# Kernel tuning notes

Hardware: AMD Instinct MI355X
Metric: run time of the kernel (lower is better)

Reference implementation:

```python
import jax, jax.numpy as jnp
import numpy as np

HIDDEN = 128
GRID = 8
NEIGH = 4.0
CELL = NEIGH / GRID


def setup_inputs() -> dict:
    key = jax.random.key(0)
    k1, k2, k3, k4 = jax.random.split(key, 4)
    B, N = 64, 64
    hidden_states = jax.random.normal(k1, (B, N, HIDDEN), dtype=jnp.float32)
    positions = jax.random.normal(k2, (B, N, 2), dtype=jnp.float32)
    fan_in = HIDDEN * GRID * GRID
    bound = 1.0 / np.sqrt(fan_in)
    W = jax.random.uniform(k3, (HIDDEN, fan_in), minval=-bound, maxval=bound, dtype=jnp.float32)
    b = jax.random.uniform(k4, (HIDDEN,), minval=-bound, maxval=bound, dtype=jnp.float32)
    return {"hidden_states": hidden_states, "positions": positions, "W": W, "b": b}


def reference(hidden_states, positions, W, b):
    B, N, H = hidden_states.shape
    G, G2 = GRID, GRID * GRID
    # rel[b, i, j] = positions[b, j] - positions[b, i]  (offset of neighbor j in agent i's frame)
    rel = positions[:, None, :, :] - positions[:, :, None, :]  # [B, N, N, 2]
    # torch .long() truncates toward zero; jnp astype(int32) does the same, and after
    # clamping to [0, G-1] this matches the original exactly.
    gx = ((rel[..., 0] + NEIGH / 2) / CELL).astype(jnp.int32).clip(0, G - 1)
    gy = ((rel[..., 1] + NEIGH / 2) / CELL).astype(jnp.int32).clip(0, G - 1)
    cell = gx * G + gy  # [B, N(i), N(j)] flat grid-cell index (gx-major, matching view order)
    # Exclude self (j == i) from pooling.
    not_self = (1.0 - jnp.eye(N, dtype=hidden_states.dtype))  # [N(i), N(j)]
    onehot = jax.nn.one_hot(cell, G2, dtype=hidden_states.dtype) * not_self[None, :, :, None]
    # Scatter-add neighbor hidden states into each agent's grid: [B, N(i), G2, H]
    grid = jnp.einsum('bijc,bjh->bich', onehot, hidden_states)
    grid_flat = grid.reshape(B, N, G2 * H)  # (gx, gy, h) flatten order == torch .view
    pooled = grid_flat @ W.T + b  # [B, N, H]
    return pooled
```

## Files before the change

kernel.cpp:

```cpp
#include <hip/hip_runtime.h>
#include <hip/hip_bf16.h>
#include <stdint.h>


typedef __attribute__((ext_vector_type(8))) short bf16x8;
typedef __attribute__((ext_vector_type(4))) float f32x4;
typedef unsigned int u32;

#define NCHUNK 8
#define CPB 8

__device__ inline unsigned short bf16bits(float x) {
    __hip_bfloat16 h = __float2bfloat16(x);
    return *reinterpret_cast<unsigned short*>(&h);
}

__global__ __launch_bounds__(512)
void gp_wconv(const float* __restrict__ W, __hip_bfloat16* __restrict__ Wb)
{
    __shared__ __attribute__((aligned(16))) __hip_bfloat16 Wl[128][136];
    const int c = blockIdx.x, t = threadIdx.x;
    #pragma unroll
    for (int q = 0; q < 8; ++q) {
        int flat = q * 512 + t;
        int ho = flat >> 5, k4 = flat & 31;
        float4 v = *(const float4*)(W + (size_t)ho * 8192 + c * 128 + k4 * 4);
        __hip_bfloat16* d = &Wl[ho][k4 * 4];
        d[0] = __float2bfloat16(v.x); d[1] = __float2bfloat16(v.y);
        d[2] = __float2bfloat16(v.z); d[3] = __float2bfloat16(v.w);
    }
    __syncthreads();
    #pragma unroll
    for (int q = 0; q < 4; ++q) {
        int flat = q * 512 + t;
        int hg = flat >> 7, ho = flat & 127;
        bf16x8 v = *(const bf16x8*)&Wl[ho][hg * 8];
        *(bf16x8*)(Wb + (size_t)c * 16384 + (size_t)flat * 8) = v;
    }
}

__global__ __launch_bounds__(256, 2)
void gp_main(const float* __restrict__ hid, const float* __restrict__ pos,
             const __hip_bfloat16* __restrict__ Wb, float* __restrict__ partial)
{
    __shared__ __attribute__((aligned(16))) __hip_bfloat16 Hs[16 * 64 * 8];
    __shared__ u32 zscr[4][1024];
    __shared__ unsigned char cellt[64 * 64];
    __shared__ float ps[128];

    const int t = threadIdx.x;
    const int b = blockIdx.x & 63, chunk = blockIdx.x >> 6;
    const int w = t >> 6, lane = t & 63;
    const int l15 = lane & 15, kg = lane >> 4;

    if (t < 128) ps[t] = pos[(size_t)b * 128 + t];
    __syncthreads();

    #pragma unroll
    for (int q = 0; q < 16; ++q) {
        int idx = q * 256 + t;
        int i = idx >> 6, j = idx & 63;
        float rx = ps[j * 2 + 0] - ps[i * 2 + 0];
        float ry = ps[j * 2 + 1] - ps[i * 2 + 1];
        int gx = (int)((rx + 2.0f) * 2.0f);
        int gy = (int)((ry + 2.0f) * 2.0f);
        gx = gx < 0 ? 0 : (gx > 7 ? 7 : gx);
        gy = gy < 0 ? 0 : (gy > 7 ? 7 : gy);
        cellt[idx] = (i == j) ? 255 : (unsigned char)(gx * 8 + gy);
    }
    #pragma unroll
    for (int q = 0; q < 4; ++q) {
        int idx = q * 256 + t;
        int hg = idx >> 6, j = idx & 63;
        const float* src = hid + ((size_t)b * 64 + j) * 128 + hg * 8;
        float4 v0 = *(const float4*)src;
        float4 v1 = *(const float4*)(src + 4);
        __hip_bfloat16* d = &Hs[(hg * 64 + j) * 8];
        d[0] = __float2bfloat16(v0.x); d[1] = __float2bfloat16(v0.y);
        d[2] = __float2bfloat16(v0.z); d[3] = __float2bfloat16(v0.w);
        d[4] = __float2bfloat16(v1.x); d[5] = __float2bfloat16(v1.y);
        d[6] = __float2bfloat16(v1.z); d[7] = __float2bfloat16(v1.w);
    }
    __syncthreads();

    bf16x8 a[4][4];
    #pragma unroll
    for (int jt = 0; jt < 4; ++jt)
        #pragma unroll
        for (int ks = 0; ks < 4; ++ks) {
            int hg = ks * 4 + kg;
            a[jt][ks] = *(const bf16x8*)&Hs[(hg * 64 + jt * 16 + l15) * 8];
        }
    uint2 cs[4][2];
    #pragma unroll
    for (int mt = 0; mt < 4; ++mt)
        #pragma unroll
        for (int ks2 = 0; ks2 < 2; ++ks2)
            cs[mt][ks2] = *(const uint2*)&cellt[(mt * 16 + l15) * 64 + ks2 * 32 + kg * 8];

    f32x4 acc[4][2];
    #pragma unroll
    for (int mt = 0; mt < 4; ++mt) {
        acc[mt][0] = (f32x4){0.f, 0.f, 0.f, 0.f};
        acc[mt][1] = (f32x4){0.f, 0.f, 0.f, 0.f};
    }

    u32* zw = &zscr[w][0];

    bf16x8 wf[2][4][2];
    {
        const __hip_bfloat16* wc = Wb + (size_t)(chunk * CPB) * 16384;
        #pragma unroll
        for (int ks = 0; ks < 4; ++ks)
            #pragma unroll
            for (int fh = 0; fh < 2; ++fh)
                wf[0][ks][fh] = *(const bf16x8*)(wc +
                    ((size_t)(ks * 4 + kg) * 128 + w * 32 + fh * 16 + l15) * 8);
    }

    #pragma unroll
    for (int cc = 0; cc < CPB; ++cc) {
        const int p = cc & 1;
        const int c = chunk * CPB + cc;

        if (cc + 1 < CPB) {
            const __hip_bfloat16* wc = Wb + (size_t)(c + 1) * 16384;
            #pragma unroll
            for (int ks = 0; ks < 4; ++ks)
                #pragma unroll
                for (int fh = 0; fh < 2; ++fh)
                    wf[p ^ 1][ks][fh] = *(const bf16x8*)(wc +
                        ((size_t)(ks * 4 + kg) * 128 + w * 32 + fh * 16 + l15) * 8);
        }

        f32x4 z[4][2];
        #pragma unroll
        for (int jt = 0; jt < 4; ++jt) {
            z[jt][0] = (f32x4){0.f, 0.f, 0.f, 0.f};
            z[jt][1] = (f32x4){0.f, 0.f, 0.f, 0.f};
        }
        #pragma unroll
        for (int ks = 0; ks < 4; ++ks)
            #pragma unroll
            for (int jt = 0; jt < 4; ++jt) {
                z[jt][0] = __builtin_amdgcn_mfma_f32_16x16x32_bf16(a[jt][ks], wf[p][ks][0], z[jt][0], 0, 0, 0);
                z[jt][1] = __builtin_amdgcn_mfma_f32_16x16x32_bf16(a[jt][ks], wf[p][ks][1], z[jt][1], 0, 0, 0);
            }

        #pragma unroll
        for (int jt = 0; jt < 4; ++jt)
            #pragma unroll
            for (int fh = 0; fh < 2; ++fh) {
                u32 p0 = (u32)bf16bits(z[jt][fh][0]) | ((u32)bf16bits(z[jt][fh][1]) << 16);
                u32 p1 = (u32)bf16bits(z[jt][fh][2]) | ((u32)bf16bits(z[jt][fh][3]) << 16);
                int X = ((jt * 2 + (kg >> 1)) & 3) << 3;
                int a32 = (((jt * 8 + kg * 2) * 32) + fh * 16 + l15) ^ X;
                zw[a32] = p0;
                zw[a32 + 32] = p1;
            }

        bf16x8 b2[2][2];
        #pragma unroll
        for (int ks2 = 0; ks2 < 2; ++ks2)
            #pragma unroll
            for (int fh = 0; fh < 2; ++fh) {
                int base = (((ks2 * 16 + kg * 4) * 32) + fh * 16 + l15) ^ (kg << 3);
                union { u32 wd[4]; bf16x8 v; } r;
                r.wd[0] = zw[base];
                r.wd[1] = zw[base + 32];
                r.wd[2] = zw[base + 64];
                r.wd[3] = zw[base + 96];
                b2[ks2][fh] = r.v;
            }

        #pragma unroll
        for (int mt = 0; mt < 4; ++mt) {
            #pragma unroll
            for (int ks2 = 0; ks2 < 2; ++ks2) {
                union { u32 wd[4]; bf16x8 v; } m;
                u32 s0 = cs[mt][ks2].x, s1 = cs[mt][ks2].y;
                #pragma unroll
                for (int k = 0; k < 4; ++k) {
                    u32 s = (k < 2) ? s0 : s1;
                    u32 b0 = (s >> ((k & 1) * 16)) & 0xFFu;
                    u32 b1 = (s >> ((k & 1) * 16 + 8)) & 0xFFu;
                    m.wd[k] = (b0 == (u32)c ? 0x3F80u : 0u) | (b1 == (u32)c ? 0x3F800000u : 0u);
                }
                acc[mt][0] = __builtin_amdgcn_mfma_f32_16x16x32_bf16(m.v, b2[ks2][0], acc[mt][0], 0, 0, 0);
                acc[mt][1] = __builtin_amdgcn_mfma_f32_16x16x32_bf16(m.v, b2[ks2][1], acc[mt][1], 0, 0, 0);
            }
        }
    }

    float* pb = partial + (((size_t)chunk * 64 + b) * 64) * 128;
    #pragma unroll
    for (int mt = 0; mt < 4; ++mt)
        #pragma unroll
        for (int fh = 0; fh < 2; ++fh)
            #pragma unroll
            for (int r = 0; r < 4; ++r) {
                int i = mt * 16 + kg * 4 + r;
                int ho = w * 32 + fh * 16 + l15;
                pb[(size_t)i * 128 + ho] = acc[mt][fh][r];
            }
}

__global__ __launch_bounds__(512)
void gp_reduce(const float* __restrict__ partial, const float* __restrict__ bias,
               float* __restrict__ out)
{
    int gid = blockIdx.x * 512 + threadIdx.x;
    int ho4 = gid & 31;
    float4 a = *(const float4*)(bias + ho4 * 4);
    #pragma unroll
    for (int ch = 0; ch < NCHUNK; ++ch) {
        float4 v = *(const float4*)(partial + (size_t)ch * 524288 + (size_t)gid * 4);
        a.x += v.x; a.y += v.y; a.z += v.z; a.w += v.w;
    }
    *(float4*)(out + (size_t)gid * 4) = a;
}

extern "C" void kernel_launch(void* const* d_in, const int* in_sizes, int n_in,
                              void* d_out, int out_size, void* d_ws, size_t ws_size,
                              hipStream_t stream)
{
    const float* hid  = (const float*)d_in[0];
    const float* pos  = (const float*)d_in[1];
    const float* W    = (const float*)d_in[2];
    const float* bias = (const float*)d_in[3];
    float* out = (float*)d_out;

    __hip_bfloat16* Wb = (__hip_bfloat16*)d_ws;
    float* partial = (float*)((char*)d_ws + (size_t)2097152);

    hipLaunchKernelGGL(gp_wconv,  dim3(64),          dim3(512), 0, stream, W, Wb);
    hipLaunchKernelGGL(gp_main,   dim3(NCHUNK * 64), dim3(256), 0, stream, hid, pos, Wb, partial);
    hipLaunchKernelGGL(gp_reduce, dim3(256),         dim3(512), 0, stream, partial, bias, out);
}
```

Baseline: 38.42 us.

## Split main kernel into single-wave blocks and hoist per-batch prep into prep kernel

Per-batch cell-index computation and hidden-state bf16 conversion move out of the main kernel into a combined prep kernel that also converts W, finer-grained. The main kernel now runs one wave per block (4096 blocks, chunk count doubled to 16), reading bf16 hidden states and cell tables from global memory, with no block-level syncs and no W double-buffering. This aims to raise parallelism and remove the redundant per-block prep. In exchange, the reduce pass reads twice as many partials and the main kernel loses its software prefetch of W.

```diff
diff --git a/kernel.cpp b/kernel.cpp
--- a/kernel.cpp
+++ b/kernel.cpp
@@ -7,96 +7,104 @@
 typedef __attribute__((ext_vector_type(4))) float f32x4;
 typedef unsigned int u32;
 
-#define NCHUNK 8
-#define CPB 8
+#define NCHUNK 16
+#define CPB 4
 
 __device__ inline unsigned short bf16bits(float x) {
     __hip_bfloat16 h = __float2bfloat16(x);
     return *reinterpret_cast<unsigned short*>(&h);
 }
 
-__global__ __launch_bounds__(512)
-void gp_wconv(const float* __restrict__ W, __hip_bfloat16* __restrict__ Wb)
-{
-    __shared__ __attribute__((aligned(16))) __hip_bfloat16 Wl[128][136];
-    const int c = blockIdx.x, t = threadIdx.x;
-    #pragma unroll
-    for (int q = 0; q < 8; ++q) {
-        int flat = q * 512 + t;
-        int ho = flat >> 5, k4 = flat & 31;
-        float4 v = *(const float4*)(W + (size_t)ho * 8192 + c * 128 + k4 * 4);
-        __hip_bfloat16* d = &Wl[ho][k4 * 4];
-        d[0] = __float2bfloat16(v.x); d[1] = __float2bfloat16(v.y);
-        d[2] = __float2bfloat16(v.z); d[3] = __float2bfloat16(v.w);
-    }
-    __syncthreads();
-    #pragma unroll
-    for (int q = 0; q < 4; ++q) {
-        int flat = q * 512 + t;
-        int hg = flat >> 7, ho = flat & 127;
-        bf16x8 v = *(const bf16x8*)&Wl[ho][hg * 8];
-        *(bf16x8*)(Wb + (size_t)c * 16384 + (size_t)flat * 8) = v;
-    }
-}
-
-__global__ __launch_bounds__(256, 2)
-void gp_main(const float* __restrict__ hid, const float* __restrict__ pos,
-             const __hip_bfloat16* __restrict__ Wb, float* __restrict__ partial)
-{
-    __shared__ __attribute__((aligned(16))) __hip_bfloat16 Hs[16 * 64 * 8];
-    __shared__ u32 zscr[4][1024];
-    __shared__ unsigned char cellt[64 * 64];
-    __shared__ float ps[128];
-
-    const int t = threadIdx.x;
-    const int b = blockIdx.x & 63, chunk = blockIdx.x >> 6;
-    const int w = t >> 6, lane = t & 63;
+__global__ __launch_bounds__(256)
+void gp_prep(const float* __restrict__ W, const float* __restrict__ pos,
+             const float* __restrict__ hid,
+             __hip_bfloat16* __restrict__ Wb,
+             unsigned char* __restrict__ cellt_g,
+             __hip_bfloat16* __restrict__ Hb)
+{
+    const int bid = blockIdx.x, t = threadIdx.x;
+    if (bid < 256) {
+        __shared__ __attribute__((aligned(16))) __hip_bfloat16 Wl[32][136];
+        const int c = bid >> 2, q = bid & 3;
+        #pragma unroll
+        for (int it = 0; it < 4; ++it) {
+            int idx = it * 256 + t;
+            int r = idx >> 5, k4 = idx & 31;
+            float4 v = *(const float4*)(W + (size_t)(q * 32 + r) * 8192 + c * 128 + k4 * 4);
+            __hip_bfloat16* d = &Wl[r][k4 * 4];
+            d[0] = __float2bfloat16(v.x); d[1] = __float2bfloat16(v.y);
+            d[2] = __float2bfloat16(v.z); d[3] = __float2bfloat16(v.w);
+        }
+        __syncthreads();
+        #pragma unroll
+        for (int it = 0; it < 2; ++it) {
+            int idx = it * 256 + t;
+            int hg = idx >> 5, hol = idx & 31;
+            bf16x8 v = *(const bf16x8*)&Wl[hol][hg * 8];
+            *(bf16x8*)(Wb + (size_t)c * 16384 + hg * 1024 + (q * 32 + hol) * 8) = v;
+        }
+    } else if (bid < 320) {
+        __shared__ float ps[128];
+        const int b = bid - 256;
+        if (t < 128) ps[t] = pos[(size_t)b * 128 + t];
+        __syncthreads();
+        #pragma unroll
+        for (int qq = 0; qq < 16; ++qq) {
+            int idx = qq * 256 + t;
+            int i = idx >> 6, j = idx & 63;
+            float rx = ps[j * 2 + 0] - ps[i * 2 + 0];
+            float ry = ps[j * 2 + 1] - ps[i * 2 + 1];
+            int gx = (int)((rx + 2.0f) * 2.0f);
+            int gy = (int)((ry + 2.0f) * 2.0f);
+            gx = gx < 0 ? 0 : (gx > 7 ? 7 : gx);
+            gy = gy < 0 ? 0 : (gy > 7 ? 7 : gy);
+            cellt_g[(size_t)b * 4096 + idx] =
+                (i == j) ? 255 : (unsigned char)(gx * 8 + gy);
+        }
+    } else {
+        const int b = bid - 320;
+        #pragma unroll
+        for (int qq = 0; qq < 8; ++qq) {
+            int idx = qq * 256 + t;
+            float4 v = *(const float4*)(hid + (size_t)b * 8192 + idx * 4);
+            union { unsigned short us[4]; uint2 u; } pk;
+            pk.us[0] = bf16bits(v.x); pk.us[1] = bf16bits(v.y);
+            pk.us[2] = bf16bits(v.z); pk.us[3] = bf16bits(v.w);
+            *(uint2*)(Hb + (size_t)b * 8192 + idx * 4) = pk.u;
+        }
+    }
+}
+
+__global__ __launch_bounds__(64, 4)
+void gp_main(const __hip_bfloat16* __restrict__ Hb,
+             const unsigned char* __restrict__ cellt_g,
+             const __hip_bfloat16* __restrict__ Wb,
+             float* __restrict__ partial)
+{
+    __shared__ u32 zscr[1024];
+
+    const int x = blockIdx.x;
+    const int w = x & 3;
+    const int b = (x >> 2) & 63;
+    const int chunk = x >> 8;
+    const int lane = threadIdx.x;
     const int l15 = lane & 15, kg = lane >> 4;
 
-    if (t < 128) ps[t] = pos[(size_t)b * 128 + t];
-    __syncthreads();
-
-    #pragma unroll
-    for (int q = 0; q < 16; ++q) {
-        int idx = q * 256 + t;
-        int i = idx >> 6, j = idx & 63;
-        float rx = ps[j * 2 + 0] - ps[i * 2 + 0];
-        float ry = ps[j * 2 + 1] - ps[i * 2 + 1];
-        int gx = (int)((rx + 2.0f) * 2.0f);
-        int gy = (int)((ry + 2.0f) * 2.0f);
-        gx = gx < 0 ? 0 : (gx > 7 ? 7 : gx);
-        gy = gy < 0 ? 0 : (gy > 7 ? 7 : gy);
-        cellt[idx] = (i == j) ? 255 : (unsigned char)(gx * 8 + gy);
-    }
-    #pragma unroll
-    for (int q = 0; q < 4; ++q) {
-        int idx = q * 256 + t;
-        int hg = idx >> 6, j = idx & 63;
-        const float* src = hid + ((size_t)b * 64 + j) * 128 + hg * 8;
-        float4 v0 = *(const float4*)src;
-        float4 v1 = *(const float4*)(src + 4);
-        __hip_bfloat16* d = &Hs[(hg * 64 + j) * 8];
-        d[0] = __float2bfloat16(v0.x); d[1] = __float2bfloat16(v0.y);
-        d[2] = __float2bfloat16(v0.z); d[3] = __float2bfloat16(v0.w);
-        d[4] = __float2bfloat16(v1.x); d[5] = __float2bfloat16(v1.y);
-        d[6] = __float2bfloat16(v1.z); d[7] = __float2bfloat16(v1.w);
-    }
-    __syncthreads();
+    uint2 cs[4][2];
+    #pragma unroll
+    for (int mt = 0; mt < 4; ++mt)
+        #pragma unroll
+        for (int ks2 = 0; ks2 < 2; ++ks2)
+            cs[mt][ks2] = *(const uint2*)(cellt_g + (size_t)b * 4096 +
+                                          (mt * 16 + l15) * 64 + ks2 * 32 + kg * 8);
 
     bf16x8 a[4][4];
     #pragma unroll
     for (int jt = 0; jt < 4; ++jt)
         #pragma unroll
-        for (int ks = 0; ks < 4; ++ks) {
-            int hg = ks * 4 + kg;
-            a[jt][ks] = *(const bf16x8*)&Hs[(hg * 64 + jt * 16 + l15) * 8];
-        }
-    uint2 cs[4][2];
-    #pragma unroll
-    for (int mt = 0; mt < 4; ++mt)
-        #pragma unroll
-        for (int ks2 = 0; ks2 < 2; ++ks2)
-            cs[mt][ks2] = *(const uint2*)&cellt[(mt * 16 + l15) * 64 + ks2 * 32 + kg * 8];
+        for (int ks = 0; ks < 4; ++ks)
+            a[jt][ks] = *(const bf16x8*)(Hb + (size_t)b * 8192 +
+                                         (jt * 16 + l15) * 128 + (ks * 4 + kg) * 8);
 
     f32x4 acc[4][2];
     #pragma unroll
@@ -105,33 +113,17 @@
         acc[mt][1] = (f32x4){0.f, 0.f, 0.f, 0.f};
     }
 
-    u32* zw = &zscr[w][0];
-
-    bf16x8 wf[2][4][2];
-    {
-        const __hip_bfloat16* wc = Wb + (size_t)(chunk * CPB) * 16384;
+    #pragma unroll
+    for (int cc = 0; cc < CPB; ++cc) {
+        const int c = chunk * CPB + cc;
+
+        bf16x8 wf[4][2];
         #pragma unroll
         for (int ks = 0; ks < 4; ++ks)
             #pragma unroll
             for (int fh = 0; fh < 2; ++fh)
-                wf[0][ks][fh] = *(const bf16x8*)(wc +
-                    ((size_t)(ks * 4 + kg) * 128 + w * 32 + fh * 16 + l15) * 8);
-    }
-
-    #pragma unroll
-    for (int cc = 0; cc < CPB; ++cc) {
-        const int p = cc & 1;
-        const int c = chunk * CPB + cc;
-
-        if (cc + 1 < CPB) {
-            const __hip_bfloat16* wc = Wb + (size_t)(c + 1) * 16384;
-            #pragma unroll
-            for (int ks = 0; ks < 4; ++ks)
-                #pragma unroll
-                for (int fh = 0; fh < 2; ++fh)
-                    wf[p ^ 1][ks][fh] = *(const bf16x8*)(wc +
-                        ((size_t)(ks * 4 + kg) * 128 + w * 32 + fh * 16 + l15) * 8);
-        }
+                wf[ks][fh] = *(const bf16x8*)(Wb + (size_t)c * 16384 +
+                    ((ks * 4 + kg) * 128 + w * 32 + fh * 16 + l15) * 8);
 
         f32x4 z[4][2];
         #pragma unroll
@@ -143,8 +135,8 @@
         for (int ks = 0; ks < 4; ++ks)
             #pragma unroll
             for (int jt = 0; jt < 4; ++jt) {
-                z[jt][0] = __builtin_amdgcn_mfma_f32_16x16x32_bf16(a[jt][ks], wf[p][ks][0], z[jt][0], 0, 0, 0);
-                z[jt][1] = __builtin_amdgcn_mfma_f32_16x16x32_bf16(a[jt][ks], wf[p][ks][1], z[jt][1], 0, 0, 0);
+                z[jt][0] = __builtin_amdgcn_mfma_f32_16x16x32_bf16(a[jt][ks], wf[ks][0], z[jt][0], 0, 0, 0);
+                z[jt][1] = __builtin_amdgcn_mfma_f32_16x16x32_bf16(a[jt][ks], wf[ks][1], z[jt][1], 0, 0, 0);
             }
 
         #pragma unroll
@@ -155,8 +147,8 @@
                 u32 p1 = (u32)bf16bits(z[jt][fh][2]) | ((u32)bf16bits(z[jt][fh][3]) << 16);
                 int X = ((jt * 2 + (kg >> 1)) & 3) << 3;
                 int a32 = (((jt * 8 + kg * 2) * 32) + fh * 16 + l15) ^ X;
-                zw[a32] = p0;
-                zw[a32 + 32] = p1;
+                zscr[a32] = p0;
+                zscr[a32 + 32] = p1;
             }
 
         bf16x8 b2[2][2];
@@ -166,10 +158,10 @@
             for (int fh = 0; fh < 2; ++fh) {
                 int base = (((ks2 * 16 + kg * 4) * 32) + fh * 16 + l15) ^ (kg << 3);
                 union { u32 wd[4]; bf16x8 v; } r;
-                r.wd[0] = zw[base];
-                r.wd[1] = zw[base + 32];
-                r.wd[2] = zw[base + 64];
-                r.wd[3] = zw[base + 96];
+                r.wd[0] = zscr[base];
+                r.wd[1] = zscr[base + 32];
+                r.wd[2] = zscr[base + 64];
+                r.wd[3] = zscr[base + 96];
                 b2[ks2][fh] = r.v;
             }
 
@@ -205,11 +197,11 @@
             }
 }
 
-__global__ __launch_bounds__(512)
+__global__ __launch_bounds__(256)
 void gp_reduce(const float* __restrict__ partial, const float* __restrict__ bias,
                float* __restrict__ out)
 {
-    int gid = blockIdx.x * 512 + threadIdx.x;
+    int gid = blockIdx.x * 256 + threadIdx.x;
     int ho4 = gid & 31;
     float4 a = *(const float4*)(bias + ho4 * 4);
     #pragma unroll
@@ -230,10 +222,16 @@
     const float* bias = (const float*)d_in[3];
     float* out = (float*)d_out;
 
-    __hip_bfloat16* Wb = (__hip_bfloat16*)d_ws;
-    float* partial = (float*)((char*)d_ws + (size_t)2097152);
-
-    hipLaunchKernelGGL(gp_wconv,  dim3(64),          dim3(512), 0, stream, W, Wb);
-    hipLaunchKernelGGL(gp_main,   dim3(NCHUNK * 64), dim3(256), 0, stream, hid, pos, Wb, partial);
-    hipLaunchKernelGGL(gp_reduce, dim3(256),         dim3(512), 0, stream, partial, bias, out);
-}
+    char* ws = (char*)d_ws;
+    __hip_bfloat16* Wb      = (__hip_bfloat16*)(ws);
+    __hip_bfloat16* Hb      = (__hip_bfloat16*)(ws + (2u << 20));
+    unsigned char*  cellt_g = (unsigned char*) (ws + (3u << 20));
+    float*          partial = (float*)         (ws + (4u << 20));
+
+    hipLaunchKernelGGL(gp_prep,   dim3(384),             dim3(256), 0, stream,
+                       W, pos, hid, Wb, cellt_g, Hb);
+    hipLaunchKernelGGL(gp_main,   dim3(NCHUNK * 64 * 4), dim3(64),  0, stream,
+                       Hb, cellt_g, Wb, partial);
+    hipLaunchKernelGGL(gp_reduce, dim3(512),             dim3(256), 0, stream,
+                       partial, bias, out);
+}
```

Result: slower. 65.40 us (+70.2%).
